# Kernel optimization log

Hardware: AMD Instinct MI355X
Metric: run time of the kernel (lower is better)

Reference implementation:

```python
import jax, jax.numpy as jnp
import numpy as np
import itertools

N_PARTICLES = 8388608
GRID_RES = 2048
BOX_SIZE = 1000.0

def _rotations_47():
    perms = list(itertools.permutations([0, 1, 2]))
    signs = list(itertools.product([1, -1], repeat=3))
    mats = []
    for s in signs:
        for p in perms:
            M = np.zeros((3, 3), np.float32)
            M[0, p[0]] = s[0]; M[1, p[1]] = s[1]; M[2, p[2]] = s[2]
            mats.append(M)
    return jnp.asarray(np.stack(mats)[1:])  # drop identity -> 47 matrices

# Analytic stand-ins for jax_cosmo background quantities (EdS-like forms).
def _Gp(a):
    return a ** 1.5

def _dGfa(a):
    return 1.5 * jnp.sqrt(a)

def _a_of_chi(chi):
    return 1.0 / (1.0 + chi / 3000.0)

def _paint_2d(pos, center, width, box_size, res):
    """CIC scatter of particles inside a z-slab onto a [res,res] density plane."""
    z = pos[:, 2]
    sel = ((z >= center - width * 0.5) & (z < center + width * 0.5)).astype(pos.dtype)
    xy = pos[:, :2] * (res / box_size)          # grid coordinates, [N,2]
    i0 = jnp.floor(xy)
    f = xy - i0                                  # CIC fractional offsets
    i0 = i0.astype(jnp.int32)
    ix0 = jnp.mod(i0[:, 0], res); iy0 = jnp.mod(i0[:, 1], res)
    ix1 = jnp.mod(i0[:, 0] + 1, res); iy1 = jnp.mod(i0[:, 1] + 1, res)
    fx, fy = f[:, 0], f[:, 1]
    flat = jnp.zeros((res * res,), dtype=pos.dtype)
    flat = flat.at[ix0 * res + iy0].add(sel * (1 - fx) * (1 - fy))
    flat = flat.at[ix1 * res + iy0].add(sel * fx * (1 - fy))
    flat = flat.at[ix0 * res + iy1].add(sel * (1 - fx) * fy)
    flat = flat.at[ix1 * res + iy1].add(sel * fx * fy)
    return flat.reshape(res, res)

def setup_inputs():
    key = jax.random.key(0)
    k1, k2 = jax.random.split(key)
    positions = jax.random.uniform(k1, (N_PARTICLES, 3), jnp.float32) * BOX_SIZE
    velocities = jax.random.normal(k2, (N_PARTICLES, 3), jnp.float32) * 2.0
    return {
        "positions": positions,
        "velocities": velocities,
        "rotations": _rotations_47(),
        "observer": jnp.zeros((3,), jnp.float32),
        "r_centers": jnp.asarray([250.0, 750.0, 1250.0, 1750.0], jnp.float32),
        "density_widths": jnp.full((4,), 500.0, jnp.float32),
        "t": jnp.float32(0.8),
        "max_comoving_distance": jnp.float32(BOX_SIZE),
        "box_size": jnp.float32(BOX_SIZE),
        "shell_idx": 2,
        "rotation_idx": 1,
        "grid_res": GRID_RES,
    }

def reference(positions, velocities, rotations, observer, r_centers, density_widths,
              t, max_comoving_distance, box_size, shell_idx, rotation_idx, grid_res):
    r_center = r_centers[shell_idx]
    width = density_widths[shell_idx]
    inside_box = r_center + width * 0.5 <= max_comoving_distance

    def inside_branch(args):
        pos, _vel = args
        return _paint_2d(pos, r_center, width, box_size, grid_res)

    def telephoto_branch(args):
        pos, vel = args
        M = rotations[rotation_idx % 47]                                   # [3,3]
        shift = jnp.floor(r_center / max_comoving_distance) * max_comoving_distance
        p_rot = (pos - observer) @ M.T                                      # rotate about observer
        z_axis = jnp.array([0.0, 0.0, 1.0], pos.dtype)
        p_shift = p_rot + z_axis * shift
        v_rot = vel @ M.T
        dist = jnp.linalg.norm(p_shift - observer, axis=-1)                 # [N]
        a_tgt = _a_of_chi(dist)[:, None]                                    # per-particle target scale factor
        ac = jnp.sqrt(t * a_tgt)
        drift = (_Gp(a_tgt) - _Gp(t)) / _dGfa(ac)
        p_drift = p_shift + drift * v_rot
        return _paint_2d(p_drift + observer, r_center, width, box_size, grid_res)

    return jax.lax.cond(inside_box, inside_branch, telephoto_branch, (positions, velocities))
```

## Files before the change

### kernel.cpp

```cpp
#include <hip/hip_runtime.h>
#include <cmath>


#define TSZ    128
#define NBKT   256
#define DEPTH  18
#define SLOTS  16
#define NTH    256
#define WPB    4
#define NBLK   480
#define NWAVES (NBLK*WPB)
#define VEC    4

__device__ __forceinline__ float fast_rcp(float x)  { return __builtin_amdgcn_rcpf(x); }
__device__ __forceinline__ float fast_sqrt(float x) { return __builtin_amdgcn_sqrtf(x); }

__device__ __forceinline__ int wrap_idx(int v, int res) {
    v += (v < 0) ? res : 0;
    v += (v < 0) ? res : 0;
    v += (v < 0) ? res : 0;
    v -= (v >= res) ? res : 0;
    v -= (v >= res) ? res : 0;
    v -= (v >= res) ? res : 0;
    if (v < 0 || v >= res) { v %= res; if (v < 0) v += res; }
    return v;
}

__device__ __forceinline__ void scatter_direct(float* __restrict__ out, int res,
                                               int gx0, int gy0, float fx, float fy) {
    int gx1 = gx0 + 1; if (gx1 >= res) gx1 = 0;
    int gy1 = gy0 + 1; if (gy1 >= res) gy1 = 0;
    atomicAdd(&out[gx0 * res + gy0], (1.0f - fx) * (1.0f - fy));
    atomicAdd(&out[gx1 * res + gy0], fx * (1.0f - fy));
    atomicAdd(&out[gx0 * res + gy1], (1.0f - fx) * fy);
    atomicAdd(&out[gx1 * res + gy1], fx * fy);
}

__device__ __forceinline__ void rec_decode(unsigned rec, int b, int tiles,
                                           int& gx, int& gy, float& fx, float& fy) {
    int tx = b / tiles, ty = b - tx * tiles;
    gx = (tx << 7) + (int)(rec >> 25);
    gy = (ty << 7) + (int)((rec >> 18) & 127u);
    fx = (float)((rec >> 9) & 511u) * (1.0f / 512.0f);
    fy = (float)(rec & 511u) * (1.0f / 512.0f);
}

struct Uni {
    float m00, m01, m02, m10, m11, m12, m20, m21, m22;
    float ox, oy, oz, shift;
    float r_lo, r_hi, t, gp_t, scale;
    int   resm1, res, tiles;
    bool  inside;
};

struct PR {
    unsigned rec, st;
    int ix0, iy0;
    float fx, fy;
    bool val;
};

__device__ __forceinline__ PR tp_compute(
    const Uni& u, unsigned dummy,
    float px, float py, float pz, float vx, float vy, float vz)
{
    float X, Y, Z;
    if (u.inside) {
        X = px; Y = py; Z = pz;
    } else {
        const float qx_ = px - u.ox, qy_ = py - u.oy, qz_ = pz - u.oz;
        float rx = u.m00 * qx_ + u.m01 * qy_ + u.m02 * qz_;
        float ry = u.m10 * qx_ + u.m11 * qy_ + u.m12 * qz_;
        float rz = u.m20 * qx_ + u.m21 * qy_ + u.m22 * qz_ + u.shift;

        const float vrx = u.m00 * vx + u.m01 * vy + u.m02 * vz;
        const float vry = u.m10 * vx + u.m11 * vy + u.m12 * vz;
        const float vrz = u.m20 * vx + u.m21 * vy + u.m22 * vz;

        const float dx = rx - u.ox, dy = ry - u.oy, dz = rz - u.oz;
        const float dist  = fast_sqrt(dx * dx + dy * dy + dz * dz);
        const float a_tgt = fast_rcp(1.0f + dist * (1.0f / 3000.0f));
        const float ac    = fast_sqrt(u.t * a_tgt);
        const float gp_a  = a_tgt * fast_sqrt(a_tgt);
        const float drift = (gp_a - u.gp_t) * fast_rcp(1.5f * fast_sqrt(ac));

        X = rx + drift * vrx + u.ox;
        Y = ry + drift * vry + u.oy;
        Z = rz + drift * vrz + u.oz;
    }
    PR o;
    o.val = (Z >= u.r_lo && Z < u.r_hi);

    const float gx = X * u.scale, gy = Y * u.scale;
    const float fgx = floorf(gx), fgy = floorf(gy);
    o.fx = gx - fgx; o.fy = gy - fgy;
    o.ix0 = ((int)fgx) & u.resm1;
    o.iy0 = ((int)fgy) & u.resm1;
    const unsigned st = (unsigned)((o.ix0 >> 7) * u.tiles + (o.iy0 >> 7));
    o.st = o.val ? st : dummy;

    unsigned qx = (unsigned)(o.fx * 512.0f + 0.5f); if (qx > 511u) qx = 511u;
    unsigned qy = (unsigned)(o.fy * 512.0f + 0.5f); if (qy > 511u) qy = 511u;
    o.rec = ((unsigned)(o.ix0 & 127) << 25) | ((unsigned)(o.iy0 & 127) << 18)
          | (qx << 9) | qy;
    return o;
}

__device__ __forceinline__ void tp_finish(
    const Uni& u, const PR& o, unsigned p,
    unsigned* __restrict__ fill, unsigned* __restrict__ buf,
    float* __restrict__ out)
{
    if (!o.val) return;
    if (p < DEPTH) buf[o.st * DEPTH + p] = o.rec;
    else { atomicSub(&fill[o.st], 1u); scatter_direct(out, u.res, o.ix0, o.iy0, o.fx, o.fy); }
}

__device__ __forceinline__ void flush_if(
    const Uni& u, const PR& o, unsigned p, unsigned w,
    unsigned* __restrict__ fill, unsigned* __restrict__ buf,
    unsigned char* __restrict__ cid,
    unsigned* __restrict__ grec, float* __restrict__ out)
{
    if (o.val && p == 15u) {
        const unsigned b = o.st;
        const unsigned c = fill[b];
        const unsigned ci = cid[b];
        if (ci == 0u) {
            const size_t dst = ((size_t)b * NWAVES + w) * SLOTS;
            #pragma unroll
            for (int i = 0; i < 16; i += 4) {
                uint4 v;
                v.x = buf[b * DEPTH + i];
                v.y = buf[b * DEPTH + i + 1];
                v.z = buf[b * DEPTH + i + 2];
                v.w = buf[b * DEPTH + i + 3];
                *(uint4*)(grec + dst + i) = v;
            }
        } else {
            for (int i = 0; i < 16; ++i) {
                int gx0, gy0; float ffx, ffy;
                rec_decode(buf[b * DEPTH + i], (int)b, u.tiles, gx0, gy0, ffx, ffy);
                scatter_direct(out, u.res, gx0, gy0, ffx, ffy);
            }
        }
        cid[b] = (unsigned char)(ci + 1u);
        const unsigned resid = c - 16u;
        for (unsigned j = 0; j < resid; ++j)
            buf[b * DEPTH + j] = buf[b * DEPTH + 16u + j];
        fill[b] = resid;
    }
}

__global__ __launch_bounds__(NTH) void tp_bin(
    const float* __restrict__ pos, const float* __restrict__ vel,
    const float* __restrict__ rotations, const float* __restrict__ observer,
    const float* __restrict__ r_centers, const float* __restrict__ widths,
    const float* __restrict__ t_p, const float* __restrict__ maxd_p,
    const float* __restrict__ box_p, const int* __restrict__ shell_p,
    const int* __restrict__ ridx_p,
    unsigned char* __restrict__ cnts, unsigned* __restrict__ grec,
    float* __restrict__ out, int res, int tiles, int n, int cpw)
{
    __shared__ unsigned fillS[WPB][NBKT + 64];
    __shared__ unsigned bufS[WPB][NBKT * DEPTH];
    __shared__ unsigned char cidS[WPB][NBKT];

    const int tid  = threadIdx.x;
    const int wv   = tid >> 6;
    const int lane = tid & 63;
    unsigned* __restrict__ fill = fillS[wv];
    unsigned* __restrict__ buf  = bufS[wv];
    unsigned char* __restrict__ cid = cidS[wv];

    for (int b = lane; b < NBKT + 64; b += 64) fill[b] = 0;
    for (int b = lane; b < NBKT; b += 64) cid[b] = 0;

    Uni u;
    {
        const int   shell    = shell_p[0];
        const float r_center = r_centers[shell];
        const float width    = widths[shell];
        const float maxd     = maxd_p[0];
        const float box      = box_p[0];
        u.t      = t_p[0];
        u.inside = (r_center + width * 0.5f) <= maxd;
        int ridx = ridx_p[0] % 47; if (ridx < 0) ridx += 47;
        const float* M = rotations + 9 * ridx;
        u.m00 = M[0]; u.m01 = M[1]; u.m02 = M[2];
        u.m10 = M[3]; u.m11 = M[4]; u.m12 = M[5];
        u.m20 = M[6]; u.m21 = M[7]; u.m22 = M[8];
        u.ox = observer[0]; u.oy = observer[1]; u.oz = observer[2];
        u.shift = floorf(r_center / maxd) * maxd;
        u.r_lo = r_center - width * 0.5f;
        u.r_hi = r_center + width * 0.5f;
        u.gp_t = u.t * sqrtf(u.t);
        u.scale = (float)res / box;
        u.resm1 = res - 1; u.res = res; u.tiles = tiles;
    }

    const unsigned w = (unsigned)(blockIdx.x * WPB + wv);
    const unsigned dummy = (unsigned)(NBKT + lane);
    const float4* __restrict__ pos4 = (const float4*)pos;
    const float4* __restrict__ vel4 = (const float4*)vel;

    for (int k = 0; k < cpw; ++k) {
        const int base = (((k * NWAVES + (int)w) * 64) + lane) * VEC;
        PR pr[4];
        if (base + VEC <= n) {
            const int q = base * 3 / 4;
            const float4 a = pos4[q], b = pos4[q + 1], c = pos4[q + 2];
            if (u.inside) {
                pr[0] = tp_compute(u, dummy, a.x, a.y, a.z, 0, 0, 0);
                pr[1] = tp_compute(u, dummy, a.w, b.x, b.y, 0, 0, 0);
                pr[2] = tp_compute(u, dummy, b.z, b.w, c.x, 0, 0, 0);
                pr[3] = tp_compute(u, dummy, c.y, c.z, c.w, 0, 0, 0);
            } else {
                const float4 d = vel4[q], e = vel4[q + 1], f = vel4[q + 2];
                pr[0] = tp_compute(u, dummy, a.x, a.y, a.z, d.x, d.y, d.z);
                pr[1] = tp_compute(u, dummy, a.w, b.x, b.y, d.w, e.x, e.y);
                pr[2] = tp_compute(u, dummy, b.z, b.w, c.x, e.z, e.w, f.x);
                pr[3] = tp_compute(u, dummy, c.y, c.z, c.w, f.y, f.z, f.w);
            }
        } else {
            #pragma unroll
            for (int j = 0; j < VEC; ++j) {
                const int i = base + j;
                const bool ok = (i >= 0) && (i < n);
                float px = 0, py = 0, pz = 0, vx = 0, vy = 0, vz = 0;
                if (ok) {
                    px = pos[3 * i]; py = pos[3 * i + 1]; pz = pos[3 * i + 2];
                    if (!u.inside) {
                        vx = vel[3 * i]; vy = vel[3 * i + 1]; vz = vel[3 * i + 2];
                    }
                }
                PR t = tp_compute(u, dummy, px, py, pz, vx, vy, vz);
                if (!ok) { t.val = false; t.st = dummy; }
                pr[j] = t;
            }
        }
        unsigned pp[4];
        #pragma unroll
        for (int j = 0; j < 4; ++j) pp[j] = atomicAdd(&fill[pr[j].st], 1u);
        #pragma unroll
        for (int j = 0; j < 4; ++j) tp_finish(u, pr[j], pp[j], fill, buf, out);
        #pragma unroll
        for (int j = 0; j < 4; ++j) flush_if(u, pr[j], pp[j], w, fill, buf, cid, grec, out);
    }

    #pragma unroll
    for (int j = 0; j < NBKT / 64; ++j) {
        const int b = lane + j * 64;
        const unsigned c = fill[b];
        const unsigned ci = cid[b];
        unsigned char cb;
        if (ci == 0u) {
            cb = (unsigned char)c;
            const size_t dst = ((size_t)b * NWAVES + w) * SLOTS;
            for (unsigned i = 0; i < c; ++i) grec[dst + i] = buf[b * DEPTH + i];
        } else {
            cb = (unsigned char)SLOTS;
            for (unsigned i = 0; i < c; ++i) {
                int gx0, gy0; float ffx, ffy;
                rec_decode(buf[b * DEPTH + i], b, u.tiles, gx0, gy0, ffx, ffy);
                scatter_direct(out, u.res, gx0, gy0, ffx, ffy);
            }
        }
        cnts[(size_t)w * NBKT + b] = cb;
    }
}

__global__ __launch_bounds__(1024) void tp_paint(
    const unsigned char* __restrict__ cnts, const unsigned* __restrict__ grec,
    float* __restrict__ out, int res, int tiles)
{
    __shared__ unsigned long long quad[4][64 * 64];
    __shared__ unsigned char cs[NWAVES];
    const int b = blockIdx.x;
    const int tx = b / tiles, ty = b - tx * tiles;

    for (int c = threadIdx.x; c < 4 * 64 * 64; c += blockDim.x)
        quad[c >> 12][c & 4095] = 0ull;
    for (int i = threadIdx.x; i < NWAVES; i += blockDim.x)
        cs[i] = cnts[(size_t)i * NBKT + b];
    __syncthreads();

    const unsigned* __restrict__ rr = grec + (size_t)b * NWAVES * SLOTS;
    const int total = NWAVES * SLOTS;
    for (int idx = threadIdx.x; idx < total; idx += blockDim.x) {
        const unsigned p = rr[idx];
        if ((idx & (SLOTS - 1)) < (int)cs[idx >> 4]) {
            const int li = (int)(p >> 25);
            const int lj = (int)((p >> 18) & 127u);
            const unsigned qx = (p >> 9) & 511u;
            const unsigned qy = p & 511u;
            const unsigned ax = 512u - qx, ay = 512u - qy;
            const unsigned long long w00 = (ax * ay + 128u) >> 8;
            const unsigned long long w01 = (ax * qy + 128u) >> 8;
            const unsigned long long w10 = (qx * ay + 128u) >> 8;
            const unsigned long long w11 = (qx * qy + 128u) >> 8;
            const unsigned long long pk = w00 | (w01 << 16) | (w10 << 32) | (w11 << 48);
            const int g = ((li & 1) << 1) | (lj & 1);
            atomicAdd(&quad[g][(li >> 1) * 64 + (lj >> 1)], pk);
        }
    }
    __syncthreads();

    for (int c = threadIdx.x; c < (TSZ + 1) * (TSZ + 1); c += blockDim.x) {
        const int i = c / (TSZ + 1), j = c - i * (TSZ + 1);
        unsigned acc = 0;
        #pragma unroll
        for (int r = 0; r < 2; ++r) {
            const int ii = i - r;
            if (ii < 0 || ii > TSZ - 1) continue;
            #pragma unroll
            for (int s = 0; s < 2; ++s) {
                const int jj = j - s;
                if (jj < 0 || jj > TSZ - 1) continue;
                const int g = ((ii & 1) << 1) | (jj & 1);
                const unsigned long long v = quad[g][(ii >> 1) * 64 + (jj >> 1)];
                acc += (unsigned)((v >> (16 * (r * 2 + s))) & 0xffffull);
            }
        }
        const float val = (float)acc * (1.0f / 1024.0f);
        int gx = tx * TSZ + i; if (gx >= res) gx -= res;
        int gy = ty * TSZ + j; if (gy >= res) gy -= res;
        float* dst = &out[gx * res + gy];
        if (i == 0 || j == 0 || i == TSZ || j == TSZ) {
            if (val != 0.0f) atomicAdd(dst, val);
        } else {
            *dst += val;
        }
    }
}

__global__ __launch_bounds__(256) void tp_direct(
    const float* __restrict__ pos, const float* __restrict__ vel,
    const float* __restrict__ rotations, const float* __restrict__ observer,
    const float* __restrict__ r_centers, const float* __restrict__ widths,
    const float* __restrict__ t_p, const float* __restrict__ maxd_p,
    const float* __restrict__ box_p, const int* __restrict__ shell_p,
    const int* __restrict__ ridx_p, float* __restrict__ out, int res, int n)
{
    int i = blockIdx.x * blockDim.x + threadIdx.x;
    if (i >= n) return;
    const int   shell    = shell_p[0];
    const float r_center = r_centers[shell];
    const float width    = widths[shell];
    const float maxd     = maxd_p[0];
    const float box      = box_p[0];
    const float t        = t_p[0];
    const bool  inside   = (r_center + width * 0.5f) <= maxd;
    int ridx = ridx_p[0] % 47; if (ridx < 0) ridx += 47;

    float px = pos[3 * i], py = pos[3 * i + 1], pz = pos[3 * i + 2];
    float X, Y, Z;
    if (inside) {
        X = px; Y = py; Z = pz;
    } else {
        const float* M = rotations + 9 * ridx;
        const float ox = observer[0], oy = observer[1], oz = observer[2];
        const float qx = px - ox, qy = py - oy, qz = pz - oz;
        float rx = M[0] * qx + M[1] * qy + M[2] * qz;
        float ry = M[3] * qx + M[4] * qy + M[5] * qz;
        float rz = M[6] * qx + M[7] * qy + M[8] * qz + floorf(r_center / maxd) * maxd;
        const float vx = vel[3 * i], vy = vel[3 * i + 1], vz = vel[3 * i + 2];
        const float vrx = M[0] * vx + M[1] * vy + M[2] * vz;
        const float vry = M[3] * vx + M[4] * vy + M[5] * vz;
        const float vrz = M[6] * vx + M[7] * vy + M[8] * vz;
        const float dx = rx - ox, dy = ry - oy, dz = rz - oz;
        const float dist  = sqrtf(dx * dx + dy * dy + dz * dz);
        const float a_tgt = 1.0f / (1.0f + dist / 3000.0f);
        const float ac    = sqrtf(t * a_tgt);
        const float drift = (a_tgt * sqrtf(a_tgt) - t * sqrtf(t)) / (1.5f * sqrtf(ac));
        X = rx + drift * vrx + ox;
        Y = ry + drift * vry + oy;
        Z = rz + drift * vrz + oz;
    }
    if (!(Z >= r_center - width * 0.5f && Z < r_center + width * 0.5f)) return;

    const float scale = (float)res / box;
    const float gx = X * scale, gy = Y * scale;
    const float fgx = floorf(gx), fgy = floorf(gy);
    scatter_direct(out, res, wrap_idx((int)fgx, res), wrap_idx((int)fgy, res),
                   gx - fgx, gy - fgy);
}

extern "C" void kernel_launch(void* const* d_in, const int* in_sizes, int n_in,
                              void* d_out, int out_size, void* d_ws, size_t ws_size,
                              hipStream_t stream) {
    const float* pos   = (const float*)d_in[0];
    const float* velv  = (const float*)d_in[1];
    const float* rot   = (const float*)d_in[2];
    const float* obs   = (const float*)d_in[3];
    const float* rc    = (const float*)d_in[4];
    const float* dw    = (const float*)d_in[5];
    const float* t     = (const float*)d_in[6];
    const float* maxd  = (const float*)d_in[7];
    const float* box   = (const float*)d_in[8];
    const int*   shell = (const int*)d_in[9];
    const int*   ridx  = (const int*)d_in[10];
    float* out = (float*)d_out;

    const int n   = in_sizes[0] / 3;
    const int res = (int)llround(sqrt((double)out_size));

    hipMemsetAsync(out, 0, (size_t)out_size * sizeof(float), stream);

    const int tiles = res / TSZ;
    const int nt2 = tiles * tiles;
    const size_t rec_bytes = (size_t)NBKT * NWAVES * SLOTS * sizeof(unsigned);
    const size_t cnt_bytes = (size_t)NWAVES * NBKT;
    const bool pow2 = res > 0 && (res & (res - 1)) == 0;

    if (!pow2 || res % TSZ != 0 || nt2 > NBKT ||
        (long long)res * res != (long long)out_size ||
        ws_size < rec_bytes + cnt_bytes) {
        tp_direct<<<(n + 255) / 256, 256, 0, stream>>>(
            pos, velv, rot, obs, rc, dw, t, maxd, box, shell, ridx, out, res, n);
        return;
    }

    unsigned* grec = (unsigned*)d_ws;
    unsigned char* cnts = (unsigned char*)d_ws + rec_bytes;

    const int per_sweep = NWAVES * 64 * VEC;
    const int cpw = (n + per_sweep - 1) / per_sweep;
    tp_bin<<<NBLK, NTH, 0, stream>>>(
        pos, velv, rot, obs, rc, dw, t, maxd, box, shell, ridx,
        cnts, grec, out, res, tiles, n, cpw);

    tp_paint<<<nt2, 1024, 0, stream>>>(cnts, grec, out, res, tiles);
}
```

Baseline: 289.2 us.

## Replace per-wave LDS staging buffers with block-shared counters writing records directly

```diff
diff --git a/kernel.cpp b/kernel.cpp
--- a/kernel.cpp
+++ b/kernel.cpp
@@ -4,11 +4,10 @@
 
 #define TSZ    128
 #define NBKT   256
-#define DEPTH  18
-#define SLOTS  16
+#define SLOTS  32
 #define NTH    256
 #define WPB    4
-#define NBLK   480
+#define NBLK   1008
 #define NWAVES (NBLK*WPB)
 #define VEC    4
 
@@ -106,52 +105,6 @@
     return o;
 }
 
-__device__ __forceinline__ void tp_finish(
-    const Uni& u, const PR& o, unsigned p,
-    unsigned* __restrict__ fill, unsigned* __restrict__ buf,
-    float* __restrict__ out)
-{
-    if (!o.val) return;
-    if (p < DEPTH) buf[o.st * DEPTH + p] = o.rec;
-    else { atomicSub(&fill[o.st], 1u); scatter_direct(out, u.res, o.ix0, o.iy0, o.fx, o.fy); }
-}
-
-__device__ __forceinline__ void flush_if(
-    const Uni& u, const PR& o, unsigned p, unsigned w,
-    unsigned* __restrict__ fill, unsigned* __restrict__ buf,
-    unsigned char* __restrict__ cid,
-    unsigned* __restrict__ grec, float* __restrict__ out)
-{
-    if (o.val && p == 15u) {
-        const unsigned b = o.st;
-        const unsigned c = fill[b];
-        const unsigned ci = cid[b];
-        if (ci == 0u) {
-            const size_t dst = ((size_t)b * NWAVES + w) * SLOTS;
-            #pragma unroll
-            for (int i = 0; i < 16; i += 4) {
-                uint4 v;
-                v.x = buf[b * DEPTH + i];
-                v.y = buf[b * DEPTH + i + 1];
-                v.z = buf[b * DEPTH + i + 2];
-                v.w = buf[b * DEPTH + i + 3];
-                *(uint4*)(grec + dst + i) = v;
-            }
-        } else {
-            for (int i = 0; i < 16; ++i) {
-                int gx0, gy0; float ffx, ffy;
-                rec_decode(buf[b * DEPTH + i], (int)b, u.tiles, gx0, gy0, ffx, ffy);
-                scatter_direct(out, u.res, gx0, gy0, ffx, ffy);
-            }
-        }
-        cid[b] = (unsigned char)(ci + 1u);
-        const unsigned resid = c - 16u;
-        for (unsigned j = 0; j < resid; ++j)
-            buf[b * DEPTH + j] = buf[b * DEPTH + 16u + j];
-        fill[b] = resid;
-    }
-}
-
 __global__ __launch_bounds__(NTH) void tp_bin(
     const float* __restrict__ pos, const float* __restrict__ vel,
     const float* __restrict__ rotations, const float* __restrict__ observer,
@@ -162,19 +115,13 @@
     unsigned char* __restrict__ cnts, unsigned* __restrict__ grec,
     float* __restrict__ out, int res, int tiles, int n, int cpw)
 {
-    __shared__ unsigned fillS[WPB][NBKT + 64];
-    __shared__ unsigned bufS[WPB][NBKT * DEPTH];
-    __shared__ unsigned char cidS[WPB][NBKT];
+    __shared__ unsigned fill[NBKT + 64];
 
     const int tid  = threadIdx.x;
     const int wv   = tid >> 6;
     const int lane = tid & 63;
-    unsigned* __restrict__ fill = fillS[wv];
-    unsigned* __restrict__ buf  = bufS[wv];
-    unsigned char* __restrict__ cid = cidS[wv];
-
-    for (int b = lane; b < NBKT + 64; b += 64) fill[b] = 0;
-    for (int b = lane; b < NBKT; b += 64) cid[b] = 0;
+
+    for (int b = tid; b < NBKT + 64; b += NTH) fill[b] = 0;
 
     Uni u;
     {
@@ -198,6 +145,8 @@
         u.scale = (float)res / box;
         u.resm1 = res - 1; u.res = res; u.tiles = tiles;
     }
+
+    __syncthreads();
 
     const unsigned w = (unsigned)(blockIdx.x * WPB + wv);
     const unsigned dummy = (unsigned)(NBKT + lane);
@@ -243,30 +192,21 @@
         #pragma unroll
         for (int j = 0; j < 4; ++j) pp[j] = atomicAdd(&fill[pr[j].st], 1u);
         #pragma unroll
-        for (int j = 0; j < 4; ++j) tp_finish(u, pr[j], pp[j], fill, buf, out);
-        #pragma unroll
-        for (int j = 0; j < 4; ++j) flush_if(u, pr[j], pp[j], w, fill, buf, cid, grec, out);
-    }
-
-    #pragma unroll
-    for (int j = 0; j < NBKT / 64; ++j) {
-        const int b = lane + j * 64;
-        const unsigned c = fill[b];
-        const unsigned ci = cid[b];
-        unsigned char cb;
-        if (ci == 0u) {
-            cb = (unsigned char)c;
-            const size_t dst = ((size_t)b * NWAVES + w) * SLOTS;
-            for (unsigned i = 0; i < c; ++i) grec[dst + i] = buf[b * DEPTH + i];
-        } else {
-            cb = (unsigned char)SLOTS;
-            for (unsigned i = 0; i < c; ++i) {
-                int gx0, gy0; float ffx, ffy;
-                rec_decode(buf[b * DEPTH + i], b, u.tiles, gx0, gy0, ffx, ffy);
-                scatter_direct(out, u.res, gx0, gy0, ffx, ffy);
+        for (int j = 0; j < 4; ++j) {
+            if (pr[j].val) {
+                if (pp[j] < SLOTS)
+                    grec[((size_t)pr[j].st * NBLK + blockIdx.x) * SLOTS + pp[j]] = pr[j].rec;
+                else
+                    scatter_direct(out, u.res, pr[j].ix0, pr[j].iy0, pr[j].fx, pr[j].fy);
             }
         }
-        cnts[(size_t)w * NBKT + b] = cb;
+    }
+
+    __syncthreads();
+    if (tid < NBKT) {
+        unsigned c = fill[tid];
+        if (c > SLOTS) c = SLOTS;
+        cnts[(size_t)blockIdx.x * NBKT + tid] = (unsigned char)c;
     }
 }
 
@@ -275,21 +215,21 @@
     float* __restrict__ out, int res, int tiles)
 {
     __shared__ unsigned long long quad[4][64 * 64];
-    __shared__ unsigned char cs[NWAVES];
+    __shared__ unsigned char cs[NBLK];
     const int b = blockIdx.x;
     const int tx = b / tiles, ty = b - tx * tiles;
 
     for (int c = threadIdx.x; c < 4 * 64 * 64; c += blockDim.x)
         quad[c >> 12][c & 4095] = 0ull;
-    for (int i = threadIdx.x; i < NWAVES; i += blockDim.x)
+    for (int i = threadIdx.x; i < NBLK; i += blockDim.x)
         cs[i] = cnts[(size_t)i * NBKT + b];
     __syncthreads();
 
-    const unsigned* __restrict__ rr = grec + (size_t)b * NWAVES * SLOTS;
-    const int total = NWAVES * SLOTS;
+    const unsigned* __restrict__ rr = grec + (size_t)b * NBLK * SLOTS;
+    const int total = NBLK * SLOTS;
     for (int idx = threadIdx.x; idx < total; idx += blockDim.x) {
         const unsigned p = rr[idx];
-        if ((idx & (SLOTS - 1)) < (int)cs[idx >> 4]) {
+        if ((idx & (SLOTS - 1)) < (int)cs[idx >> 5]) {
             const int li = (int)(p >> 25);
             const int lj = (int)((p >> 18) & 127u);
             const unsigned qx = (p >> 9) & 511u;
@@ -409,8 +349,8 @@
 
     const int tiles = res / TSZ;
     const int nt2 = tiles * tiles;
-    const size_t rec_bytes = (size_t)NBKT * NWAVES * SLOTS * sizeof(unsigned);
-    const size_t cnt_bytes = (size_t)NWAVES * NBKT;
+    const size_t rec_bytes = (size_t)NBKT * NBLK * SLOTS * sizeof(unsigned);
+    const size_t cnt_bytes = (size_t)NBLK * NBKT;
     const bool pow2 = res > 0 && (res & (res - 1)) == 0;
 
     if (!pow2 || res % TSZ != 0 || nt2 > NBKT ||
```

Measured after the change: 344.7 us. 19.2% more time.
